# Kernel tuning notes

Hardware: AMD Instinct MI355X
Metric: run time of the kernel (lower is better)

## Reference

```python
import jax, jax.numpy as jnp
import numpy as np

B, Q, C_IN, C_OUT, S, NH = 4, 4096, 256, 256, 8, 8
H_FEAT, W_FEAT = 128, 128


def grid_sample_bilinear(img, grid):
    """torch.nn.functional.grid_sample, mode='bilinear', padding_mode='zeros', align_corners=False.
    img: [B, C, H, W]; grid: [B, Hg, Wg, 2] with (x, y) in [-1, 1]. Returns [B, C, Hg, Wg]."""
    b, c, h, w = img.shape
    gx = (grid[..., 0] + 1.0) * (w * 0.5) - 0.5
    gy = (grid[..., 1] + 1.0) * (h * 0.5) - 0.5
    x0f = jnp.floor(gx)
    y0f = jnp.floor(gy)
    x0 = x0f.astype(jnp.int32)
    y0 = y0f.astype(jnp.int32)
    wx1 = (gx - x0f)[:, None]  # [B,1,Hg,Wg]
    wy1 = (gy - y0f)[:, None]
    img_flat = img.reshape(b, c, h * w)

    def corner(xi, yi):
        inb = ((xi >= 0) & (xi < w) & (yi >= 0) & (yi < h)).astype(img.dtype)
        idx = jnp.clip(yi, 0, h - 1) * w + jnp.clip(xi, 0, w - 1)
        v = jax.vmap(lambda im, ix: im[:, ix.reshape(-1)])(img_flat, idx)  # [B,C,Hg*Wg]
        return v.reshape(b, c, *xi.shape[1:]) * inb[:, None]

    v00 = corner(x0, y0)
    v01 = corner(x0 + 1, y0)
    v10 = corner(x0, y0 + 1)
    v11 = corner(x0 + 1, y0 + 1)
    return (v00 * (1 - wx1) * (1 - wy1) + v01 * wx1 * (1 - wy1)
            + v10 * (1 - wx1) * wy1 + v11 * wx1 * wy1)


def setup_inputs() -> dict:
    key = jax.random.key(0)
    ks = jax.random.split(key, 16)
    sc = 0.02
    return {
        "queries": jax.random.normal(ks[0], (B, Q, C_IN), jnp.float32),
        "keys": jax.random.normal(ks[1], (B, C_IN, H_FEAT, W_FEAT), jnp.float32),
        "values": jax.random.normal(ks[2], (B, C_IN, H_FEAT, W_FEAT), jnp.float32),
        "W_loc": jax.random.normal(ks[3], (C_IN, S * 2), jnp.float32) * sc,
        "b_loc": jnp.zeros((S * 2,), jnp.float32),
        "W_q": jax.random.normal(ks[4], (C_IN, C_OUT), jnp.float32) * sc,
        "b_q": jnp.zeros((C_OUT,), jnp.float32),
        "W_k": jax.random.normal(ks[5], (C_OUT, C_IN), jnp.float32) * sc,
        "b_k": jnp.zeros((C_OUT,), jnp.float32),
        "W_v": jax.random.normal(ks[6], (C_OUT, C_IN), jnp.float32) * sc,
        "b_v": jnp.zeros((C_OUT,), jnp.float32),
        "W_o": jax.random.normal(ks[7], (C_OUT, C_OUT), jnp.float32) * sc,
        "b_o": jnp.zeros((C_OUT,), jnp.float32),
    }


def reference(queries, keys, values, W_loc, b_loc, W_q, b_q, W_k, b_k, W_v, b_v, W_o, b_o):
    b, q, _ = queries.shape
    d = C_OUT // NH
    # predicted sampling locations in [-1, 1]: [B, Q, S, 2]
    loc = jnp.tanh(queries @ W_loc + b_loc).reshape(b, q, S, 2)
    # query projection -> [B, Q, NH, d]
    qh = (queries @ W_q + b_q).reshape(b, q, NH, d)
    # 1x1 conv projections of feature maps
    k_proj = jnp.einsum('oc,bchw->bohw', W_k, keys) + b_k[None, :, None, None]
    v_proj = jnp.einsum('oc,bchw->bohw', W_v, values) + b_v[None, :, None, None]
    # deformable sampling: [B, C_OUT, Q, S] -> [B, Q, NH, d, S]
    ks_ = grid_sample_bilinear(k_proj, loc).transpose(0, 2, 1, 3).reshape(b, q, NH, d, S)
    vs_ = grid_sample_bilinear(v_proj, loc).transpose(0, 2, 1, 3).reshape(b, q, NH, d, S)
    # per-query attention over S sampled points (note: scale uses full out_channels)
    attn = jnp.einsum('bqhd,bqhds->bqhs', qh, ks_) / np.sqrt(C_OUT).astype(np.float32)
    attn = jax.nn.softmax(attn, axis=-1)
    out = jnp.einsum('bqhds,bqhs->bqhd', vs_, attn).reshape(b, q, C_OUT)
    return out @ W_o + b_o
```

## Files before the change

### kernel.cpp

```cpp
#include <hip/hip_runtime.h>
#include <hip/hip_bf16.h>

#define NB 4
#define NQ 4096
#define CI 256
#define CO 256
#define NS 8
#define HFEAT 128
#define WFEAT 128
#define NPIX (HFEAT * WFEAT)

typedef short bf16x8 __attribute__((ext_vector_type(8)));
typedef float f32x4 __attribute__((ext_vector_type(4)));

__device__ __forceinline__ unsigned short f2b(float x) {
    union { float f; unsigned u; } v; v.f = x;
    unsigned r = v.u + 0x7fff + ((v.u >> 16) & 1);
    return (unsigned short)(r >> 16);
}
__device__ __forceinline__ float b2f(unsigned short x) {
    union { unsigned u; float f; } v; v.u = ((unsigned)x) << 16;
    return v.f;
}
__device__ __forceinline__ void b2f2(unsigned u, float& a, float& b) {
    union { unsigned x; float f; } va, vb;
    va.x = u << 16;
    vb.x = u & 0xffff0000u;
    a = va.f; b = vb.f;
}
__device__ __forceinline__ unsigned cvtpk(float a, float b) {
    unsigned r;
    asm("v_cvt_pk_bf16_f32 %0, %1, %2" : "=v"(r) : "v"(a), "v"(b));
    return r;
}
__device__ __forceinline__ void gload16(const void* g, void* l) {
    __builtin_amdgcn_global_load_lds((const __attribute__((address_space(1))) void*)g,
                                     (__attribute__((address_space(3))) void*)l, 16, 0, 0);
}

__global__ __launch_bounds__(256) void k_prep_w(const float* __restrict__ Wk,
                                                const float* __restrict__ Wv,
                                                const float* __restrict__ Wq,
                                                const float* __restrict__ Wo,
                                                unsigned short* __restrict__ out) {
    int mat = blockIdx.y;
    int base = blockIdx.x * 1024 + threadIdx.x * 4;
    const float* src = (mat == 0) ? Wk : (mat == 1) ? Wv : (mat == 2) ? Wq : Wo;
    unsigned short* dst = out + (size_t)mat * 65536;
    if (mat < 2) {
#pragma unroll
        for (int i = 0; i < 4; ++i) dst[base + i] = f2b(src[base + i]);
    } else {
#pragma unroll
        for (int i = 0; i < 4; ++i) {
            int oi = base + i;
            int o = oi >> 8, c = oi & 255;
            dst[oi] = f2b(src[c * 256 + o]);
        }
    }
}

__global__ __launch_bounds__(256) void k_qprep(const float* __restrict__ q,
                                               const float* __restrict__ Wl,
                                               const float* __restrict__ bl,
                                               float* __restrict__ loc,
                                               unsigned short* __restrict__ qbf) {
    __shared__ float qs[32][260];
    __shared__ float wlt[16][260];
    int t = threadIdx.x;
    int row0 = blockIdx.x * 32;
    {
        int rr = t >> 6;
        int c4 = (t & 63) * 4;
#pragma unroll
        for (int i = 0; i < 8; ++i) {
            int r = i * 4 + rr;
            *reinterpret_cast<float4*>(&qs[r][c4]) =
                *reinterpret_cast<const float4*>(q + (size_t)(row0 + r) * CI + c4);
        }
    }
    {
        int c = t;
#pragma unroll
        for (int col = 0; col < 16; ++col) wlt[col][c] = Wl[c * 16 + col];
    }
    __syncthreads();
    {
        int rr = t >> 3, cc = (t & 7) * 32;
        unsigned short* dst = qbf + (size_t)(row0 + rr) * CI + cc;
#pragma unroll
        for (int i = 0; i < 4; ++i) {
            uint4 pk4;
            pk4.x = cvtpk(qs[rr][cc + i * 8 + 0], qs[rr][cc + i * 8 + 1]);
            pk4.y = cvtpk(qs[rr][cc + i * 8 + 2], qs[rr][cc + i * 8 + 3]);
            pk4.z = cvtpk(qs[rr][cc + i * 8 + 4], qs[rr][cc + i * 8 + 5]);
            pk4.w = cvtpk(qs[rr][cc + i * 8 + 6], qs[rr][cc + i * 8 + 7]);
            *reinterpret_cast<uint4*>(dst + i * 8) = pk4;
        }
    }
    int r = t & 31;
    int cg = t >> 5;
    float a0 = bl[cg], a1 = bl[cg + 8];
    for (int c4 = 0; c4 < 256; c4 += 4) {
        float4 qv = *reinterpret_cast<const float4*>(&qs[r][c4]);
        float4 w0 = *reinterpret_cast<const float4*>(&wlt[cg][c4]);
        float4 w1 = *reinterpret_cast<const float4*>(&wlt[cg + 8][c4]);
        a0 = fmaf(qv.x, w0.x, a0); a0 = fmaf(qv.y, w0.y, a0);
        a0 = fmaf(qv.z, w0.z, a0); a0 = fmaf(qv.w, w0.w, a0);
        a1 = fmaf(qv.x, w1.x, a1); a1 = fmaf(qv.y, w1.y, a1);
        a1 = fmaf(qv.z, w1.z, a1); a1 = fmaf(qv.w, w1.w, a1);
    }
    loc[(size_t)(row0 + r) * 16 + cg] = tanhf(a0);
    loc[(size_t)(row0 + r) * 16 + cg + 8] = tanhf(a1);
}

template <int OUT_BF16>
__global__ __launch_bounds__(256) void k_gemm(const unsigned short* __restrict__ A,
                                              const unsigned short* __restrict__ Bt,
                                              const float* __restrict__ bias,
                                              void* __restrict__ outp) {
    __shared__ unsigned short As[128][32];
    __shared__ unsigned short Bs[128][32];
    int t = threadIdx.x;
    int w = t >> 6, l = t & 63;
    int bm = blockIdx.x >> 1, bc = blockIdx.x & 1;
    int m0 = bm * 128, n0 = bc * 128;
    int wr = w >> 1, wc = w & 1;

    f32x4 acc[4][4];
#pragma unroll
    for (int n = 0; n < 4; ++n) {
        float bv = bias[n0 + wc * 64 + n * 16 + (l & 15)];
#pragma unroll
        for (int m = 0; m < 4; ++m) acc[m][n] = f32x4{bv, bv, bv, bv};
    }

    int ar = wr * 64 + (l & 15);
    int br = wc * 64 + (l & 15);
    int kq = (l >> 4) * 8;
    int srow = (l >> 2);
    int scol = (l & 3) * 8;

    for (int kk = 0; kk < 8; ++kk) {
        int k0 = kk * 32;
#pragma unroll
        for (int j = 0; j < 2; ++j) {
            int row = w * 32 + j * 16 + srow;
            gload16(A + (size_t)(m0 + row) * CI + k0 + scol, &As[w * 32 + j * 16][0]);
            gload16(Bt + (size_t)(n0 + row) * CI + k0 + scol, &Bs[w * 32 + j * 16][0]);
        }
        __syncthreads();
        bf16x8 af[4], bfr[4];
#pragma unroll
        for (int m = 0; m < 4; ++m) af[m] = *reinterpret_cast<const bf16x8*>(&As[ar + m * 16][kq]);
#pragma unroll
        for (int n = 0; n < 4; ++n) bfr[n] = *reinterpret_cast<const bf16x8*>(&Bs[br + n * 16][kq]);
#pragma unroll
        for (int m = 0; m < 4; ++m)
#pragma unroll
            for (int n = 0; n < 4; ++n)
                acc[m][n] = __builtin_amdgcn_mfma_f32_16x16x32_bf16(af[m], bfr[n], acc[m][n], 0, 0, 0);
        __syncthreads();
    }

    int rbase = m0 + wr * 64 + (l >> 4) * 4;
    int cbase = n0 + wc * 64 + (l & 15);
#pragma unroll
    for (int m = 0; m < 4; ++m)
#pragma unroll
        for (int n = 0; n < 4; ++n)
#pragma unroll
            for (int r = 0; r < 4; ++r) {
                size_t row = rbase + m * 16 + r;
                size_t col = cbase + n * 16;
                if (OUT_BF16)
                    ((unsigned short*)outp)[row * CO + col] = f2b(acc[m][n][r]);
                else
                    ((float*)outp)[row * CO + col] = acc[m][n][r];
            }
}

__global__ __launch_bounds__(256) void k_proj(const float* __restrict__ keys,
                                              const float* __restrict__ values,
                                              const unsigned short* __restrict__ wbuf,
                                              const float* __restrict__ bK,
                                              const float* __restrict__ bV,
                                              unsigned short* __restrict__ kp,
                                              unsigned short* __restrict__ vp) {
    __shared__ unsigned short As[128][40];
    __shared__ unsigned short Bs[2][128][32];
    int blk = ((blockIdx.x & 7) << 8) | (blockIdx.x >> 3);
    int map = blk >> 10;
    int rem = blk & 1023;
    int b = rem >> 8;
    int rem2 = rem & 255;
    int pix0 = (rem2 >> 1) * 128;
    int o0 = (rem2 & 1) * 128;
    const float* X = (map ? values : keys) + (size_t)b * (CI * NPIX);
    const unsigned short* W = wbuf + (size_t)map * 65536;
    const float* bias = map ? bV : bK;
    unsigned short* outp = (map ? vp : kp) + (size_t)b * (NPIX * CO);

    int t = threadIdx.x;
    int w = t >> 6, l = t & 63;
    int wr = w >> 1, wc = w & 1;

    f32x4 acc[4][4];
#pragma unroll
    for (int n = 0; n < 4; ++n) {
        float bv = bias[o0 + wc * 64 + n * 16 + (l & 15)];
#pragma unroll
        for (int m = 0; m < 4; ++m) acc[m][n] = f32x4{bv, bv, bv, bv};
    }

    int cp0 = t >> 5;
    int pxl = 4 * (t & 31);
    int fx = ((t & 31) ^ ((t & 31) >> 2)) & 3;
    int colA = cp0 ^ (fx << 2);
    int colB = (cp0 + 8) ^ (fx << 2);
    const float* Xp = X + pix0 + pxl;

    int srow = l >> 2, scol = (l & 3) * 8;

    int ar = wr * 64 + (l & 15);
    int br = wc * 64 + (l & 15);
    int g = l >> 4;
    int kq = g * 8;

    float4 fa0, fa1, fa2, fa3;

#define LOADA(kk)                                                         \
    {                                                                     \
        const float* p_ = Xp + (size_t)((kk) * 32 + 2 * cp0) * NPIX;      \
        fa0 = *(const float4*)(p_);                                       \
        fa1 = *(const float4*)(p_ + NPIX);                                \
        fa2 = *(const float4*)(p_ + 16 * NPIX);                           \
        fa3 = *(const float4*)(p_ + 17 * NPIX);                           \
    }
#define WRITEA()                                                          \
    {                                                                     \
        const float* q0_ = (const float*)&fa0;                            \
        const float* q1_ = (const float*)&fa1;                            \
        const float* q2_ = (const float*)&fa2;                            \
        const float* q3_ = (const float*)&fa3;                            \
        _Pragma("unroll")                                                 \
        for (int j = 0; j < 4; ++j) {                                     \
            unsigned d0_ = (unsigned)f2b(q0_[j]) | ((unsigned)f2b(q1_[j]) << 16); \
            unsigned d1_ = (unsigned)f2b(q2_[j]) | ((unsigned)f2b(q3_[j]) << 16); \
            unsigned* rp_ = (unsigned*)&As[pxl + j][0];                   \
            rp_[colA] = d0_;                                              \
            rp_[colB] = d1_;                                              \
        }                                                                 \
    }
#define LOADB(kk, buf)                                                    \
    {                                                                     \
        int k0_ = (kk) * 32;                                              \
        _Pragma("unroll")                                                 \
        for (int j = 0; j < 2; ++j) {                                     \
            int row_ = w * 32 + j * 16;                                   \
            gload16(W + (size_t)(o0 + row_ + srow) * CI + k0_ + scol,     \
                    &Bs[buf][row_][0]);                                   \
        }                                                                 \
    }

    LOADA(0);
    LOADB(0, 0);
    WRITEA();
    __syncthreads();

    for (int kk = 0; kk < 8; ++kk) {
        if (kk < 7) {
            LOADA(kk + 1);
            LOADB(kk + 1, (kk + 1) & 1);
        }
        bf16x8 af[4], bfr[4];
#pragma unroll
        for (int m = 0; m < 4; ++m) {
            int p = ar + m * 16;
            int gm = (g ^ (((p >> 2) ^ (p >> 4)) & 3)) * 8;
            af[m] = *reinterpret_cast<const bf16x8*>(&As[p][gm]);
        }
#pragma unroll
        for (int n = 0; n < 4; ++n)
            bfr[n] = *reinterpret_cast<const bf16x8*>(&Bs[kk & 1][br + n * 16][kq]);
#pragma unroll
        for (int m = 0; m < 4; ++m)
#pragma unroll
            for (int n = 0; n < 4; ++n)
                acc[m][n] = __builtin_amdgcn_mfma_f32_16x16x32_bf16(af[m], bfr[n], acc[m][n], 0, 0, 0);
        __syncthreads();
        if (kk < 7) {
            WRITEA();
            __syncthreads();
        }
    }

    int rbase = wr * 64 + (l >> 4) * 4;
    int cbase = o0 + wc * 64 + (l & 15);
#pragma unroll
    for (int m = 0; m < 4; ++m)
#pragma unroll
        for (int n = 0; n < 4; ++n)
#pragma unroll
            for (int r = 0; r < 4; ++r) {
                size_t row = (size_t)pix0 + rbase + m * 16 + r;
                size_t col = cbase + n * 16;
                outp[row * CO + col] = f2b(acc[m][n][r]);
            }
#undef LOADA
#undef WRITEA
#undef LOADB
}

__global__ __launch_bounds__(256) void k_attn(const unsigned short* __restrict__ kp,
                                              const unsigned short* __restrict__ vp,
                                              const unsigned short* __restrict__ qh,
                                              const float* __restrict__ loc,
                                              unsigned short* __restrict__ aout) {
    int t = threadIdx.x;
    int wv = t >> 6, l = t & 63;
    int blk = blockIdx.x;
    int xcd = blk & 7;
    int b = xcd >> 1;
    int idx = ((blk >> 3) << 1) | (xcd & 1);
    int bq = (b << 12) | (idx << 2) | wv;

    float qv[4];
    {
        uint2 qr = *reinterpret_cast<const uint2*>(qh + (size_t)bq * CO + l * 4);
        b2f2(qr.x, qv[0], qv[1]);
        b2f2(qr.y, qv[2], qv[3]);
    }
    const unsigned short* kb = kp + (size_t)b * NPIX * CO + l * 4;
    const unsigned short* vb = vp + (size_t)b * NPIX * CO + l * 4;
    const float* lq = loc + (size_t)bq * (NS * 2);

    int i00[NS];
    float w00[NS], w01[NS], w10[NS], w11[NS];
    unsigned msks = 0;
#pragma unroll
    for (int s = 0; s < NS; ++s) {
        float gx = (lq[2 * s] + 1.f) * (WFEAT * 0.5f) - 0.5f;
        float gy = (lq[2 * s + 1] + 1.f) * (HFEAT * 0.5f) - 0.5f;
        float x0f = floorf(gx), y0f = floorf(gy);
        int x0 = (int)x0f, y0 = (int)y0f;
        float wx1 = gx - x0f, wy1 = gy - y0f;
        float wx0 = 1.f - wx1, wy0 = 1.f - wy1;
        w00[s] = wx0 * wy0; w01[s] = wx1 * wy0;
        w10[s] = wx0 * wy1; w11[s] = wx1 * wy1;
        unsigned xa = (unsigned)x0 < WFEAT, xb = (unsigned)(x0 + 1) < WFEAT;
        unsigned ya = (unsigned)y0 < HFEAT, yb = (unsigned)(y0 + 1) < HFEAT;
        msks |= ((xa & ya) | ((xb & ya) << 1) | ((xa & yb) << 2) | ((xb & yb) << 3)) << (4 * s);
        i00[s] = (y0 * WFEAT + x0) * CO;
    }

    uint2 cr[NS][4];
#pragma unroll
    for (int s = 0; s < NS; ++s) {
        uint2 z = make_uint2(0u, 0u);
        cr[s][0] = z; cr[s][1] = z; cr[s][2] = z; cr[s][3] = z;
        unsigned m4 = msks >> (4 * s);
        if (m4 & 1) cr[s][0] = *(const uint2*)(kb + i00[s]);
        if (m4 & 2) cr[s][1] = *(const uint2*)(kb + i00[s] + CO);
        if (m4 & 4) cr[s][2] = *(const uint2*)(kb + i00[s] + WFEAT * CO);
        if (m4 & 8) cr[s][3] = *(const uint2*)(kb + i00[s] + (WFEAT + 1) * CO);
    }
    float lg[NS];
#pragma unroll
    for (int s = 0; s < NS; ++s) {
        float d[4];
#pragma unroll
        for (int c = 0; c < 4; ++c) {
            float a0, a1, a2, a3;
            b2f2(cr[s][c].x, a0, a1);
            b2f2(cr[s][c].y, a2, a3);
            d[c] = fmaf(qv[0], a0, fmaf(qv[1], a1, fmaf(qv[2], a2, qv[3] * a3)));
        }
        float p = fmaf(d[0], w00[s], fmaf(d[1], w01[s], fmaf(d[2], w10[s], d[3] * w11[s])));
        p += __shfl_xor(p, 1);
        p += __shfl_xor(p, 2);
        p += __shfl_xor(p, 4);
        lg[s] = p * 0.0625f;
    }
    float mx = fmaxf(fmaxf(fmaxf(lg[0], lg[1]), fmaxf(lg[2], lg[3])),
                     fmaxf(fmaxf(lg[4], lg[5]), fmaxf(lg[6], lg[7])));
    float ws[NS];
    float sum = 0.f;
#pragma unroll
    for (int s = 0; s < NS; ++s) { ws[s] = __expf(lg[s] - mx); sum += ws[s]; }
    float inv = 1.f / sum;
#pragma unroll
    for (int s = 0; s < NS; ++s) ws[s] *= inv;

#pragma unroll
    for (int s = 0; s < NS; ++s) {
        uint2 z = make_uint2(0u, 0u);
        cr[s][0] = z; cr[s][1] = z; cr[s][2] = z; cr[s][3] = z;
        unsigned m4 = msks >> (4 * s);
        if (m4 & 1) cr[s][0] = *(const uint2*)(vb + i00[s]);
        if (m4 & 2) cr[s][1] = *(const uint2*)(vb + i00[s] + CO);
        if (m4 & 4) cr[s][2] = *(const uint2*)(vb + i00[s] + WFEAT * CO);
        if (m4 & 8) cr[s][3] = *(const uint2*)(vb + i00[s] + (WFEAT + 1) * CO);
    }
    float o0 = 0.f, o1 = 0.f, o2 = 0.f, o3 = 0.f;
#pragma unroll
    for (int s = 0; s < NS; ++s) {
        float f0 = ws[s] * w00[s], f1 = ws[s] * w01[s];
        float f2 = ws[s] * w10[s], f3 = ws[s] * w11[s];
        float a0, a1, a2, a3;
        b2f2(cr[s][0].x, a0, a1); b2f2(cr[s][0].y, a2, a3);
        o0 = fmaf(f0, a0, o0); o1 = fmaf(f0, a1, o1);
        o2 = fmaf(f0, a2, o2); o3 = fmaf(f0, a3, o3);
        b2f2(cr[s][1].x, a0, a1); b2f2(cr[s][1].y, a2, a3);
        o0 = fmaf(f1, a0, o0); o1 = fmaf(f1, a1, o1);
        o2 = fmaf(f1, a2, o2); o3 = fmaf(f1, a3, o3);
        b2f2(cr[s][2].x, a0, a1); b2f2(cr[s][2].y, a2, a3);
        o0 = fmaf(f2, a0, o0); o1 = fmaf(f2, a1, o1);
        o2 = fmaf(f2, a2, o2); o3 = fmaf(f2, a3, o3);
        b2f2(cr[s][3].x, a0, a1); b2f2(cr[s][3].y, a2, a3);
        o0 = fmaf(f3, a0, o0); o1 = fmaf(f3, a1, o1);
        o2 = fmaf(f3, a2, o2); o3 = fmaf(f3, a3, o3);
    }

    uint2 pk;
    pk.x = cvtpk(o0, o1);
    pk.y = cvtpk(o2, o3);
    *reinterpret_cast<uint2*>(aout + (size_t)bq * CO + l * 4) = pk;
}

extern "C" void kernel_launch(void* const* d_in, const int* in_sizes, int n_in,
                              void* d_out, int out_size, void* d_ws, size_t ws_size,
                              hipStream_t stream) {
    (void)in_sizes; (void)n_in; (void)out_size; (void)ws_size;
    const float* queries = (const float*)d_in[0];
    const float* keys    = (const float*)d_in[1];
    const float* values  = (const float*)d_in[2];
    const float* W_loc   = (const float*)d_in[3];
    const float* b_loc   = (const float*)d_in[4];
    const float* W_q     = (const float*)d_in[5];
    const float* b_q     = (const float*)d_in[6];
    const float* W_k     = (const float*)d_in[7];
    const float* b_k     = (const float*)d_in[8];
    const float* W_v     = (const float*)d_in[9];
    const float* b_v     = (const float*)d_in[10];
    const float* W_o     = (const float*)d_in[11];
    const float* b_o     = (const float*)d_in[12];
    float* out = (float*)d_out;

    char* ws = (char*)d_ws;
    unsigned short* kp   = (unsigned short*)(ws);
    unsigned short* vp   = (unsigned short*)(ws + 33554432);
    unsigned short* qbf  = (unsigned short*)(ws + 67108864);
    unsigned short* aout = (unsigned short*)(ws + 67108864);
    unsigned short* qh   = (unsigned short*)(ws + 75497472);
    float* locb          = (float*)(ws + 83886080);
    unsigned short* wbuf = (unsigned short*)(ws + 84934656);

    k_prep_w<<<dim3(64, 4), 256, 0, stream>>>(W_k, W_v, W_q, W_o, wbuf);
    k_qprep<<<dim3(512), 256, 0, stream>>>(queries, W_loc, b_loc, locb, qbf);
    k_gemm<1><<<dim3(256), 256, 0, stream>>>(qbf, wbuf + 131072, b_q, qh);
    k_proj<<<dim3(2048), 256, 0, stream>>>(keys, values, wbuf, b_k, b_v, kp, vp);
    k_attn<<<dim3(NB * NQ / 4), 256, 0, stream>>>(kp, vp, qh, locb, aout);
    k_gemm<0><<<dim3(256), 256, 0, stream>>>(aout, wbuf + 196608, b_o, out);
}
```

Baseline: 118.2 us.

## Retile k_proj GEMM to 256x256 tiles with 512 threads and K-chunk 64

Restructures the key/value 1x1-conv projection kernel. Each block now computes 256 pixels by all 256 output channels using 8 waves, so each fp32 input pixel column is loaded and converted once, not once per output half. It stages A and B in double-buffered padded LDS tiles with 64-wide K chunks, which cuts the main loop to 4 iterations with a single barrier each. The cost is a much larger LDS footprint (about 147KB per block, relying on gfx950's larger LDS) and one block per CU. It also drops the XOR swizzle in favor of row padding.

```diff
diff --git a/kernel.cpp b/kernel.cpp
--- a/kernel.cpp
+++ b/kernel.cpp
@@ -180,22 +180,22 @@
             }
 }
 
-__global__ __launch_bounds__(256) void k_proj(const float* __restrict__ keys,
+__global__ __launch_bounds__(512) void k_proj(const float* __restrict__ keys,
                                               const float* __restrict__ values,
                                               const unsigned short* __restrict__ wbuf,
                                               const float* __restrict__ bK,
                                               const float* __restrict__ bV,
                                               unsigned short* __restrict__ kp,
                                               unsigned short* __restrict__ vp) {
-    __shared__ unsigned short As[128][40];
-    __shared__ unsigned short Bs[2][128][32];
-    int blk = ((blockIdx.x & 7) << 8) | (blockIdx.x >> 3);
-    int map = blk >> 10;
-    int rem = blk & 1023;
-    int b = rem >> 8;
-    int rem2 = rem & 255;
-    int pix0 = (rem2 >> 1) * 128;
-    int o0 = (rem2 & 1) * 128;
+    __shared__ unsigned short As[2][256][72];
+    __shared__ unsigned short Bs[2][256][72];
+
+    int bid = blockIdx.x;
+    int blk = ((bid & 7) << 6) | (bid >> 3);
+    int map = blk >> 8;
+    int b = (blk >> 6) & 3;
+    int px0 = (blk & 63) << 8;
+
     const float* X = (map ? values : keys) + (size_t)b * (CI * NPIX);
     const unsigned short* W = wbuf + (size_t)map * 65536;
     const float* bias = map ? bV : bK;
@@ -203,113 +203,118 @@
 
     int t = threadIdx.x;
     int w = t >> 6, l = t & 63;
-    int wr = w >> 1, wc = w & 1;
-
-    f32x4 acc[4][4];
-#pragma unroll
-    for (int n = 0; n < 4; ++n) {
-        float bv = bias[o0 + wc * 64 + n * 16 + (l & 15)];
+    int lm = l & 15, lg = l >> 4;
+    int wpx = (w & 3) * 64;
+    int wo = (w >> 2) * 128;
+
+    int cpair = t >> 4;
+    int pxl = (t & 15) * 2;
+    int bo = t >> 1;
+    int bh = (t & 1) * 32;
+
+    f32x4 acc[4][8];
+#pragma unroll
+    for (int n = 0; n < 8; ++n) {
+        float bv = bias[wo + n * 16 + lm];
 #pragma unroll
         for (int m = 0; m < 4; ++m) acc[m][n] = f32x4{bv, bv, bv, bv};
     }
 
-    int cp0 = t >> 5;
-    int pxl = 4 * (t & 31);
-    int fx = ((t & 31) ^ ((t & 31) >> 2)) & 3;
-    int colA = cp0 ^ (fx << 2);
-    int colB = (cp0 + 8) ^ (fx << 2);
-    const float* Xp = X + pix0 + pxl;
-
-    int srow = l >> 2, scol = (l & 3) * 8;
-
-    int ar = wr * 64 + (l & 15);
-    int br = wc * 64 + (l & 15);
-    int g = l >> 4;
-    int kq = g * 8;
-
-    float4 fa0, fa1, fa2, fa3;
-
-#define LOADA(kk)                                                         \
-    {                                                                     \
-        const float* p_ = Xp + (size_t)((kk) * 32 + 2 * cp0) * NPIX;      \
-        fa0 = *(const float4*)(p_);                                       \
-        fa1 = *(const float4*)(p_ + NPIX);                                \
-        fa2 = *(const float4*)(p_ + 16 * NPIX);                           \
-        fa3 = *(const float4*)(p_ + 17 * NPIX);                           \
-    }
-#define WRITEA()                                                          \
-    {                                                                     \
-        const float* q0_ = (const float*)&fa0;                            \
-        const float* q1_ = (const float*)&fa1;                            \
-        const float* q2_ = (const float*)&fa2;                            \
-        const float* q3_ = (const float*)&fa3;                            \
-        _Pragma("unroll")                                                 \
-        for (int j = 0; j < 4; ++j) {                                     \
-            unsigned d0_ = (unsigned)f2b(q0_[j]) | ((unsigned)f2b(q1_[j]) << 16); \
-            unsigned d1_ = (unsigned)f2b(q2_[j]) | ((unsigned)f2b(q3_[j]) << 16); \
-            unsigned* rp_ = (unsigned*)&As[pxl + j][0];                   \
-            rp_[colA] = d0_;                                              \
-            rp_[colB] = d1_;                                              \
-        }                                                                 \
-    }
-#define LOADB(kk, buf)                                                    \
-    {                                                                     \
-        int k0_ = (kk) * 32;                                              \
-        _Pragma("unroll")                                                 \
-        for (int j = 0; j < 2; ++j) {                                     \
-            int row_ = w * 32 + j * 16;                                   \
-            gload16(W + (size_t)(o0 + row_ + srow) * CI + k0_ + scol,     \
-                    &Bs[buf][row_][0]);                                   \
-        }                                                                 \
-    }
-
-    LOADA(0);
-    LOADB(0, 0);
-    WRITEA();
+    float2 fa[8], fb[8];
+    uint4 wv0, wv1, wv2, wv3;
+
+#define BLOAD(cc)                                                            \
+    {                                                                        \
+        const uint4* q_ = reinterpret_cast<const uint4*>(                    \
+            W + (size_t)bo * CI + (cc) * 64 + bh);                           \
+        wv0 = q_[0];                                                         \
+        wv1 = q_[1];                                                         \
+        wv2 = q_[2];                                                         \
+        wv3 = q_[3];                                                         \
+    }
+#define BWRITE(cc, buf)                                                      \
+    {                                                                        \
+        uint4* d_ = reinterpret_cast<uint4*>(&Bs[buf][bo][bh]);              \
+        d_[0] = wv0;                                                         \
+        d_[1] = wv1;                                                         \
+        d_[2] = wv2;                                                         \
+        d_[3] = wv3;                                                         \
+    }
+#define ALOAD(cc)                                                            \
+    {                                                                        \
+        const float* p0_ = X + (size_t)((cc) * 64 + 2 * cpair) * NPIX + px0 + pxl; \
+        const float* p1_ = p0_ + NPIX;                                       \
+        _Pragma("unroll")                                                    \
+        for (int j = 0; j < 8; ++j) {                                        \
+            fa[j] = *reinterpret_cast<const float2*>(p0_ + 32 * j);          \
+            fb[j] = *reinterpret_cast<const float2*>(p1_ + 32 * j);          \
+        }                                                                    \
+    }
+#define AWRITE(cc, buf)                                                      \
+    {                                                                        \
+        _Pragma("unroll")                                                    \
+        for (int j = 0; j < 8; ++j) {                                        \
+            int px_ = 32 * j + pxl;                                          \
+            ((unsigned*)&As[buf][px_][0])[cpair] = cvtpk(fa[j].x, fb[j].x);  \
+            ((unsigned*)&As[buf][px_ + 1][0])[cpair] = cvtpk(fa[j].y, fb[j].y); \
+        }                                                                    \
+    }
+#define COMPUTE(buf)                                                         \
+    {                                                                        \
+        _Pragma("unroll")                                                    \
+        for (int ks = 0; ks < 2; ++ks) {                                     \
+            bf16x8 af[4], bfr[8];                                            \
+            _Pragma("unroll")                                                \
+            for (int m = 0; m < 4; ++m)                                      \
+                af[m] = *reinterpret_cast<const bf16x8*>(                    \
+                    &As[buf][wpx + m * 16 + lm][ks * 32 + lg * 8]);          \
+            _Pragma("unroll")                                                \
+            for (int n = 0; n < 8; ++n)                                      \
+                bfr[n] = *reinterpret_cast<const bf16x8*>(                   \
+                    &Bs[buf][wo + n * 16 + lm][ks * 32 + lg * 8]);           \
+            _Pragma("unroll")                                                \
+            for (int m = 0; m < 4; ++m)                                      \
+                _Pragma("unroll")                                            \
+                for (int n = 0; n < 8; ++n)                                  \
+                    acc[m][n] = __builtin_amdgcn_mfma_f32_16x16x32_bf16(     \
+                        af[m], bfr[n], acc[m][n], 0, 0, 0);                  \
+        }                                                                    \
+    }
+
+    BLOAD(0);
+    ALOAD(0);
+    BWRITE(0, 0);
+    AWRITE(0, 0);
     __syncthreads();
 
-    for (int kk = 0; kk < 8; ++kk) {
-        if (kk < 7) {
-            LOADA(kk + 1);
-            LOADB(kk + 1, (kk + 1) & 1);
-        }
-        bf16x8 af[4], bfr[4];
-#pragma unroll
-        for (int m = 0; m < 4; ++m) {
-            int p = ar + m * 16;
-            int gm = (g ^ (((p >> 2) ^ (p >> 4)) & 3)) * 8;
-            af[m] = *reinterpret_cast<const bf16x8*>(&As[p][gm]);
-        }
-#pragma unroll
-        for (int n = 0; n < 4; ++n)
-            bfr[n] = *reinterpret_cast<const bf16x8*>(&Bs[kk & 1][br + n * 16][kq]);
-#pragma unroll
-        for (int m = 0; m < 4; ++m)
-#pragma unroll
-            for (int n = 0; n < 4; ++n)
-                acc[m][n] = __builtin_amdgcn_mfma_f32_16x16x32_bf16(af[m], bfr[n], acc[m][n], 0, 0, 0);
+#pragma unroll
+    for (int cc = 0; cc < 4; ++cc) {
+        int buf = cc & 1;
+        if (cc < 3) {
+            BLOAD(cc + 1);
+            ALOAD(cc + 1);
+            BWRITE(cc + 1, buf ^ 1);
+        }
+        COMPUTE(buf);
+        if (cc < 3) AWRITE(cc + 1, buf ^ 1);
         __syncthreads();
-        if (kk < 7) {
-            WRITEA();
-            __syncthreads();
-        }
-    }
-
-    int rbase = wr * 64 + (l >> 4) * 4;
-    int cbase = o0 + wc * 64 + (l & 15);
+    }
+
 #pragma unroll
     for (int m = 0; m < 4; ++m)
 #pragma unroll
-        for (int n = 0; n < 4; ++n)
+        for (int n = 0; n < 8; ++n)
 #pragma unroll
             for (int r = 0; r < 4; ++r) {
-                size_t row = (size_t)pix0 + rbase + m * 16 + r;
-                size_t col = cbase + n * 16;
-                outp[row * CO + col] = f2b(acc[m][n][r]);
+                int px_ = px0 + wpx + m * 16 + lg * 4 + r;
+                int col = wo + n * 16 + lm;
+                outp[(size_t)px_ * CO + col] = f2b(acc[m][n][r]);
             }
-#undef LOADA
-#undef WRITEA
-#undef LOADB
+#undef BLOAD
+#undef BWRITE
+#undef ALOAD
+#undef AWRITE
+#undef COMPUTE
 }
 
 __global__ __launch_bounds__(256) void k_attn(const unsigned short* __restrict__ kp,
@@ -459,7 +464,7 @@
     k_prep_w<<<dim3(64, 4), 256, 0, stream>>>(W_k, W_v, W_q, W_o, wbuf);
     k_qprep<<<dim3(512), 256, 0, stream>>>(queries, W_loc, b_loc, locb, qbf);
     k_gemm<1><<<dim3(256), 256, 0, stream>>>(qbf, wbuf + 131072, b_q, qh);
-    k_proj<<<dim3(2048), 256, 0, stream>>>(keys, values, wbuf, b_k, b_v, kp, vp);
+    k_proj<<<dim3(512), 512, 0, stream>>>(keys, values, wbuf, b_k, b_v, kp, vp);
     k_attn<<<dim3(NB * NQ / 4), 256, 0, stream>>>(kp, vp, qh, locb, aout);
     k_gemm<0><<<dim3(256), 256, 0, stream>>>(aout, wbuf + 196608, b_o, out);
 }
```

Result: slower. 132.6 us (+12.2%).

## Restructure k_proj to compute full 256 output channels per 128-pixel tile

Applied to the files above, without the earlier changes.

The 1x1-conv projection kernel now uses 512-thread blocks that each compute all 256 output channels for a 128-pixel tile. Before, two blocks each produced 128 channels, so every fp32 feature tile was read twice from global memory. Raw fp32 features are loaded into shared memory with async global-to-LDS copies and converted to bf16 when the MFMA operands are built. The output tile is transposed so each lane writes packed 4-channel bf16 stores instead of scalar ones. In exchange the software double-buffering is dropped, so each K-step waits on its loads with no prefetch overlap, and the Xs column reads may cause LDS bank conflicts.

```diff
diff --git a/kernel.cpp b/kernel.cpp
--- a/kernel.cpp
+++ b/kernel.cpp
@@ -180,22 +180,22 @@
             }
 }
 
-__global__ __launch_bounds__(256) void k_proj(const float* __restrict__ keys,
+__global__ __launch_bounds__(512) void k_proj(const float* __restrict__ keys,
                                               const float* __restrict__ values,
                                               const unsigned short* __restrict__ wbuf,
                                               const float* __restrict__ bK,
                                               const float* __restrict__ bV,
                                               unsigned short* __restrict__ kp,
                                               unsigned short* __restrict__ vp) {
-    __shared__ unsigned short As[128][40];
-    __shared__ unsigned short Bs[2][128][32];
-    int blk = ((blockIdx.x & 7) << 8) | (blockIdx.x >> 3);
-    int map = blk >> 10;
-    int rem = blk & 1023;
-    int b = rem >> 8;
-    int rem2 = rem & 255;
-    int pix0 = (rem2 >> 1) * 128;
-    int o0 = (rem2 & 1) * 128;
+    __shared__ unsigned short Ws[256][40];
+    __shared__ float Xs[32][128];
+
+    int bid = blockIdx.x;
+    int L = ((bid & 7) << 7) | (bid >> 3);
+    int map = L >> 9;
+    int b = (L >> 7) & 3;
+    int px0 = (L & 127) << 7;
+
     const float* X = (map ? values : keys) + (size_t)b * (CI * NPIX);
     const unsigned short* W = wbuf + (size_t)map * 65536;
     const float* bias = map ? bV : bK;
@@ -203,113 +203,73 @@
 
     int t = threadIdx.x;
     int w = t >> 6, l = t & 63;
-    int wr = w >> 1, wc = w & 1;
+    int wp = w & 1;
+    int woq = w >> 1;
+    int lm = l & 15, lg = l >> 4;
 
     f32x4 acc[4][4];
 #pragma unroll
-    for (int n = 0; n < 4; ++n) {
-        float bv = bias[o0 + wc * 64 + n * 16 + (l & 15)];
-#pragma unroll
-        for (int m = 0; m < 4; ++m) acc[m][n] = f32x4{bv, bv, bv, bv};
-    }
-
-    int cp0 = t >> 5;
-    int pxl = 4 * (t & 31);
-    int fx = ((t & 31) ^ ((t & 31) >> 2)) & 3;
-    int colA = cp0 ^ (fx << 2);
-    int colB = (cp0 + 8) ^ (fx << 2);
-    const float* Xp = X + pix0 + pxl;
-
-    int srow = l >> 2, scol = (l & 3) * 8;
-
-    int ar = wr * 64 + (l & 15);
-    int br = wc * 64 + (l & 15);
-    int g = l >> 4;
-    int kq = g * 8;
-
-    float4 fa0, fa1, fa2, fa3;
-
-#define LOADA(kk)                                                         \
-    {                                                                     \
-        const float* p_ = Xp + (size_t)((kk) * 32 + 2 * cp0) * NPIX;      \
-        fa0 = *(const float4*)(p_);                                       \
-        fa1 = *(const float4*)(p_ + NPIX);                                \
-        fa2 = *(const float4*)(p_ + 16 * NPIX);                           \
-        fa3 = *(const float4*)(p_ + 17 * NPIX);                           \
-    }
-#define WRITEA()                                                          \
-    {                                                                     \
-        const float* q0_ = (const float*)&fa0;                            \
-        const float* q1_ = (const float*)&fa1;                            \
-        const float* q2_ = (const float*)&fa2;                            \
-        const float* q3_ = (const float*)&fa3;                            \
-        _Pragma("unroll")                                                 \
-        for (int j = 0; j < 4; ++j) {                                     \
-            unsigned d0_ = (unsigned)f2b(q0_[j]) | ((unsigned)f2b(q1_[j]) << 16); \
-            unsigned d1_ = (unsigned)f2b(q2_[j]) | ((unsigned)f2b(q3_[j]) << 16); \
-            unsigned* rp_ = (unsigned*)&As[pxl + j][0];                   \
-            rp_[colA] = d0_;                                              \
-            rp_[colB] = d1_;                                              \
-        }                                                                 \
-    }
-#define LOADB(kk, buf)                                                    \
-    {                                                                     \
-        int k0_ = (kk) * 32;                                              \
-        _Pragma("unroll")                                                 \
-        for (int j = 0; j < 2; ++j) {                                     \
-            int row_ = w * 32 + j * 16;                                   \
-            gload16(W + (size_t)(o0 + row_ + srow) * CI + k0_ + scol,     \
-                    &Bs[buf][row_][0]);                                   \
-        }                                                                 \
-    }
-
-    LOADA(0);
-    LOADB(0, 0);
-    WRITEA();
-    __syncthreads();
-
-    for (int kk = 0; kk < 8; ++kk) {
-        if (kk < 7) {
-            LOADA(kk + 1);
-            LOADB(kk + 1, (kk + 1) & 1);
-        }
+    for (int m = 0; m < 4; ++m) {
+        int ob = woq * 64 + m * 16 + lg * 4;
+        float4 bv = *reinterpret_cast<const float4*>(bias + ob);
+#pragma unroll
+        for (int n = 0; n < 4; ++n) acc[m][n] = f32x4{bv.x, bv.y, bv.z, bv.w};
+    }
+
+    int wrow = t >> 1;
+    int wh = (t & 1) * 16;
+    int xpx = (l & 31) * 4;
+    int xlr = l >> 5;
+
+    for (int cc = 0; cc < 8; ++cc) {
+#pragma unroll
+        for (int j = 0; j < 2; ++j) {
+            int row = w * 4 + 2 * j;
+            gload16(X + (size_t)(cc * 32 + row + xlr) * NPIX + px0 + xpx, &Xs[row][0]);
+        }
+        {
+            const uint4* s = reinterpret_cast<const uint4*>(W + (size_t)wrow * CI + cc * 32 + wh);
+            uint4 a = s[0], bq4 = s[1];
+            uint4* d = reinterpret_cast<uint4*>(&Ws[wrow][wh]);
+            d[0] = a;
+            d[1] = bq4;
+        }
+        __syncthreads();
+
         bf16x8 af[4], bfr[4];
 #pragma unroll
-        for (int m = 0; m < 4; ++m) {
-            int p = ar + m * 16;
-            int gm = (g ^ (((p >> 2) ^ (p >> 4)) & 3)) * 8;
-            af[m] = *reinterpret_cast<const bf16x8*>(&As[p][gm]);
-        }
-#pragma unroll
-        for (int n = 0; n < 4; ++n)
-            bfr[n] = *reinterpret_cast<const bf16x8*>(&Bs[kk & 1][br + n * 16][kq]);
+        for (int m = 0; m < 4; ++m)
+            af[m] = *reinterpret_cast<const bf16x8*>(&Ws[woq * 64 + m * 16 + lm][lg * 8]);
+#pragma unroll
+        for (int n = 0; n < 4; ++n) {
+            int px = wp * 64 + n * 16 + lm;
+            union { uint4 u; bf16x8 h; } pk;
+            pk.u.x = cvtpk(Xs[lg * 8 + 0][px], Xs[lg * 8 + 1][px]);
+            pk.u.y = cvtpk(Xs[lg * 8 + 2][px], Xs[lg * 8 + 3][px]);
+            pk.u.z = cvtpk(Xs[lg * 8 + 4][px], Xs[lg * 8 + 5][px]);
+            pk.u.w = cvtpk(Xs[lg * 8 + 6][px], Xs[lg * 8 + 7][px]);
+            bfr[n] = pk.h;
+        }
 #pragma unroll
         for (int m = 0; m < 4; ++m)
 #pragma unroll
             for (int n = 0; n < 4; ++n)
                 acc[m][n] = __builtin_amdgcn_mfma_f32_16x16x32_bf16(af[m], bfr[n], acc[m][n], 0, 0, 0);
         __syncthreads();
-        if (kk < 7) {
-            WRITEA();
-            __syncthreads();
-        }
-    }
-
-    int rbase = wr * 64 + (l >> 4) * 4;
-    int cbase = o0 + wc * 64 + (l & 15);
-#pragma unroll
-    for (int m = 0; m < 4; ++m)
-#pragma unroll
-        for (int n = 0; n < 4; ++n)
-#pragma unroll
-            for (int r = 0; r < 4; ++r) {
-                size_t row = (size_t)pix0 + rbase + m * 16 + r;
-                size_t col = cbase + n * 16;
-                outp[row * CO + col] = f2b(acc[m][n][r]);
-            }
-#undef LOADA
-#undef WRITEA
-#undef LOADB
+    }
+
+#pragma unroll
+    for (int m = 0; m < 4; ++m) {
+        int ob = woq * 64 + m * 16 + lg * 4;
+#pragma unroll
+        for (int n = 0; n < 4; ++n) {
+            int px = px0 + wp * 64 + n * 16 + lm;
+            uint2 pk;
+            pk.x = cvtpk(acc[m][n][0], acc[m][n][1]);
+            pk.y = cvtpk(acc[m][n][2], acc[m][n][3]);
+            *reinterpret_cast<uint2*>(outp + (size_t)px * CO + ob) = pk;
+        }
+    }
 }
 
 __global__ __launch_bounds__(256) void k_attn(const unsigned short* __restrict__ kp,
@@ -459,7 +419,7 @@
     k_prep_w<<<dim3(64, 4), 256, 0, stream>>>(W_k, W_v, W_q, W_o, wbuf);
     k_qprep<<<dim3(512), 256, 0, stream>>>(queries, W_loc, b_loc, locb, qbf);
     k_gemm<1><<<dim3(256), 256, 0, stream>>>(qbf, wbuf + 131072, b_q, qh);
-    k_proj<<<dim3(2048), 256, 0, stream>>>(keys, values, wbuf, b_k, b_v, kp, vp);
+    k_proj<<<dim3(1024), 512, 0, stream>>>(keys, values, wbuf, b_k, b_v, kp, vp);
     k_attn<<<dim3(NB * NQ / 4), 256, 0, stream>>>(kp, vp, qh, locb, aout);
     k_gemm<0><<<dim3(256), 256, 0, stream>>>(aout, wbuf + 196608, b_o, out);
 }
```

Result: slower. 133.8 us (+13.2%).
